# Performance work log

Measured on AMD Instinct MI355X. Metric: run time of the kernel, lower is better.

The kernel has to match this reference:

```python
import jax, jax.numpy as jnp
import numpy as np

B = 16384          # number of bags (offsets length)
L = 50             # indices per bag
N = B * L          # total flat indices
NUM_EMB = 10_000_000
DIM = 3


def setup_inputs() -> dict:
    key = jax.random.key(0)
    k_idx, k0, k1, k2 = jax.random.split(key, 4)
    eb_input = jax.random.randint(k_idx, (N,), 0, NUM_EMB, dtype=jnp.int64 if jax.config.jax_enable_x64 else jnp.int32)
    eb_offset = (jnp.arange(B) * L).astype(eb_input.dtype)  # sorted, starts at 0
    # 3 distinct tables (groups share one module object each in the original)
    table0 = jax.random.normal(k0, (NUM_EMB, DIM), dtype=jnp.float32)
    table1 = jax.random.normal(k1, (NUM_EMB, DIM), dtype=jnp.float32)
    table2 = jax.random.normal(k2, (NUM_EMB, DIM), dtype=jnp.float32)
    return {"eb_input": eb_input, "eb_offset": eb_offset,
            "table0": table0, "table1": table1, "table2": table2}


def _bag_sum(table, idx, seg_ids, num_bags):
    # gather rows then segment-sum -> EmbeddingBag(mode='sum')
    return jax.ops.segment_sum(table[idx], seg_ids, num_segments=num_bags)


def reference(eb_input, eb_offset, table0, table1, table2):
    n = eb_input.shape[0]
    num_bags = eb_offset.shape[0]
    # map each flat index position to its bag id
    seg_ids = jnp.searchsorted(eb_offset, jnp.arange(n, dtype=eb_offset.dtype), side='right') - 1
    p0 = _bag_sum(table0, eb_input, seg_ids, num_bags)  # [B, 3]
    p1 = _bag_sum(table1, eb_input, seg_ids, num_bags)
    p2 = _bag_sum(table2, eb_input, seg_ids, num_bags)
    # groups repeat the same bag 5 / 10 / 6 times, then cat along dim 0
    out = jnp.concatenate([
        jnp.tile(p0, (5, 1)),   # [5B, 3]
        jnp.tile(p1, (10, 1)),  # [10B, 3]
        jnp.tile(p2, (6, 1)),   # [6B, 3]
    ], axis=0)                   # [21B, 3]
    return out
```

## Files before the change

### kernel.cpp

```cpp
#include <hip/hip_runtime.h>


__device__ __forceinline__ float wave_reduce_sum(float v) {
#pragma unroll
    for (int off = 32; off > 0; off >>= 1)
        v += __shfl_down(v, off, 64);
    return v;
}

__global__ __launch_bounds__(256) void bag_sum_kernel(
    const int* __restrict__ eb_input,
    const int* __restrict__ eb_offset,
    const float* __restrict__ t0,
    const float* __restrict__ t1,
    const float* __restrict__ t2,
    float* __restrict__ out,
    int N, int B)
{
    const int wave = (blockIdx.x * blockDim.x + threadIdx.x) >> 6;
    const int lane = threadIdx.x & 63;
    if (wave >= B) return;

    const int start = eb_offset[wave];
    const int end   = (wave + 1 < B) ? eb_offset[wave + 1] : N;

    float s0x = 0.f, s0y = 0.f, s0z = 0.f;
    float s1x = 0.f, s1y = 0.f, s1z = 0.f;
    float s2x = 0.f, s2y = 0.f, s2z = 0.f;

    for (int i = start + lane; i < end; i += 64) {
        const long long j = (long long)eb_input[i] * 3;
        const float* __restrict__ p0 = t0 + j;
        const float* __restrict__ p1 = t1 + j;
        const float* __restrict__ p2 = t2 + j;
        s0x += p0[0]; s0y += p0[1]; s0z += p0[2];
        s1x += p1[0]; s1y += p1[1]; s1z += p1[2];
        s2x += p2[0]; s2y += p2[1]; s2z += p2[2];
    }

    s0x = wave_reduce_sum(s0x); s0y = wave_reduce_sum(s0y); s0z = wave_reduce_sum(s0z);
    s1x = wave_reduce_sum(s1x); s1y = wave_reduce_sum(s1y); s1z = wave_reduce_sum(s1z);
    s2x = wave_reduce_sum(s2x); s2y = wave_reduce_sum(s2y); s2z = wave_reduce_sum(s2z);

    if (lane == 0) {
        const size_t b = (size_t)wave;
        float* o0 = out + b * 3;
        float* o1 = out + ((size_t)5  * B + b) * 3;
        float* o2 = out + ((size_t)15 * B + b) * 3;
        o0[0] = s0x; o0[1] = s0y; o0[2] = s0z;
        o1[0] = s1x; o1[1] = s1y; o1[2] = s1z;
        o2[0] = s2x; o2[1] = s2y; o2[2] = s2z;
    }
}

__global__ __launch_bounds__(256) void tile_kernel(float* __restrict__ out, int B)
{
    const int r = blockIdx.x * blockDim.x + threadIdx.x;
    const int total = 18 * B;
    if (r >= total) return;

    size_t dst, src;
    if (r < 4 * B) {
        dst = (size_t)B + r;
        src = (size_t)(r % B);
    } else if (r < 13 * B) {
        const int q = r - 4 * B;
        dst = (size_t)6 * B + q;
        src = (size_t)5 * B + (q % B);
    } else {
        const int q = r - 13 * B;
        dst = (size_t)16 * B + q;
        src = (size_t)15 * B + (q % B);
    }

    const float* __restrict__ s = out + src * 3;
    float* __restrict__ d = out + dst * 3;
    const float a = s[0], b = s[1], c = s[2];
    d[0] = a; d[1] = b; d[2] = c;
}

extern "C" void kernel_launch(void* const* d_in, const int* in_sizes, int n_in,
                              void* d_out, int out_size, void* d_ws, size_t ws_size,
                              hipStream_t stream)
{
    const int*   eb_input  = (const int*)d_in[0];
    const int*   eb_offset = (const int*)d_in[1];
    const float* t0        = (const float*)d_in[2];
    const float* t1        = (const float*)d_in[3];
    const float* t2        = (const float*)d_in[4];
    float*       out       = (float*)d_out;

    const int N = in_sizes[0];
    const int B = in_sizes[1];

    const int blocksA = (B + 3) / 4;
    bag_sum_kernel<<<blocksA, 256, 0, stream>>>(eb_input, eb_offset, t0, t1, t2, out, N, B);

    const int totalRows = 18 * B;
    const int blocksB = (totalRows + 255) / 256;
    tile_kernel<<<blocksB, 256, 0, stream>>>(out, B);
}
```

Measured before the change: 59.19 us.

## Fuse bag-sum and tiling into one kernel with half-wave per bag

Merges the gather/sum kernel and the separate tile-copy kernel into a single launch. Each half-wave (32 lanes) now handles one bag, which suits the 50-index bags better than a full 64-lane wave. A butterfly xor reduction leaves the sum in every lane, so 21 lanes each write one replicated output row directly. This removes the second launch and the read-back of the output for tiling. Index math moves to 32-bit unsigned byte offsets, which overflow if index*12 exceeds 4 GB (fine for 10M rows).

```diff
diff --git a/kernel.cpp b/kernel.cpp
--- a/kernel.cpp
+++ b/kernel.cpp
@@ -1,14 +1,7 @@
 #include <hip/hip_runtime.h>
 
 
-__device__ __forceinline__ float wave_reduce_sum(float v) {
-#pragma unroll
-    for (int off = 32; off > 0; off >>= 1)
-        v += __shfl_down(v, off, 64);
-    return v;
-}
-
-__global__ __launch_bounds__(256) void bag_sum_kernel(
+__global__ __launch_bounds__(256) void bag_fused_kernel(
     const int* __restrict__ eb_input,
     const int* __restrict__ eb_offset,
     const float* __restrict__ t0,
@@ -17,66 +10,51 @@
     float* __restrict__ out,
     int N, int B)
 {
-    const int wave = (blockIdx.x * blockDim.x + threadIdx.x) >> 6;
+    const int wid  = (blockIdx.x * blockDim.x + threadIdx.x) >> 6;
     const int lane = threadIdx.x & 63;
-    if (wave >= B) return;
+    const int l5   = lane & 31;
+    const int b    = wid * 2 + (lane >> 5);
+    if (b >= B) return;
 
-    const int start = eb_offset[wave];
-    const int end   = (wave + 1 < B) ? eb_offset[wave + 1] : N;
+    const int start = eb_offset[b];
+    const int end   = (b + 1 < B) ? eb_offset[b + 1] : N;
 
     float s0x = 0.f, s0y = 0.f, s0z = 0.f;
     float s1x = 0.f, s1y = 0.f, s1z = 0.f;
     float s2x = 0.f, s2y = 0.f, s2z = 0.f;
 
-    for (int i = start + lane; i < end; i += 64) {
-        const long long j = (long long)eb_input[i] * 3;
-        const float* __restrict__ p0 = t0 + j;
-        const float* __restrict__ p1 = t1 + j;
-        const float* __restrict__ p2 = t2 + j;
+    for (int i = start + l5; i < end; i += 32) {
+        const unsigned idx = (unsigned)eb_input[i];
+        const size_t byteoff = (size_t)(idx * 12u);
+        const float* __restrict__ p0 = (const float*)((const char*)t0 + byteoff);
+        const float* __restrict__ p1 = (const float*)((const char*)t1 + byteoff);
+        const float* __restrict__ p2 = (const float*)((const char*)t2 + byteoff);
         s0x += p0[0]; s0y += p0[1]; s0z += p0[2];
         s1x += p1[0]; s1y += p1[1]; s1z += p1[2];
         s2x += p2[0]; s2y += p2[1]; s2z += p2[2];
     }
 
-    s0x = wave_reduce_sum(s0x); s0y = wave_reduce_sum(s0y); s0z = wave_reduce_sum(s0z);
-    s1x = wave_reduce_sum(s1x); s1y = wave_reduce_sum(s1y); s1z = wave_reduce_sum(s1z);
-    s2x = wave_reduce_sum(s2x); s2y = wave_reduce_sum(s2y); s2z = wave_reduce_sum(s2z);
-
-    if (lane == 0) {
-        const size_t b = (size_t)wave;
-        float* o0 = out + b * 3;
-        float* o1 = out + ((size_t)5  * B + b) * 3;
-        float* o2 = out + ((size_t)15 * B + b) * 3;
-        o0[0] = s0x; o0[1] = s0y; o0[2] = s0z;
-        o1[0] = s1x; o1[1] = s1y; o1[2] = s1z;
-        o2[0] = s2x; o2[1] = s2y; o2[2] = s2z;
-    }
-}
-
-__global__ __launch_bounds__(256) void tile_kernel(float* __restrict__ out, int B)
-{
-    const int r = blockIdx.x * blockDim.x + threadIdx.x;
-    const int total = 18 * B;
-    if (r >= total) return;
-
-    size_t dst, src;
-    if (r < 4 * B) {
-        dst = (size_t)B + r;
-        src = (size_t)(r % B);
-    } else if (r < 13 * B) {
-        const int q = r - 4 * B;
-        dst = (size_t)6 * B + q;
-        src = (size_t)5 * B + (q % B);
-    } else {
-        const int q = r - 13 * B;
-        dst = (size_t)16 * B + q;
-        src = (size_t)15 * B + (q % B);
+#pragma unroll
+    for (int off = 16; off > 0; off >>= 1) {
+        s0x += __shfl_xor(s0x, off, 64);
+        s0y += __shfl_xor(s0y, off, 64);
+        s0z += __shfl_xor(s0z, off, 64);
+        s1x += __shfl_xor(s1x, off, 64);
+        s1y += __shfl_xor(s1y, off, 64);
+        s1z += __shfl_xor(s1z, off, 64);
+        s2x += __shfl_xor(s2x, off, 64);
+        s2y += __shfl_xor(s2y, off, 64);
+        s2z += __shfl_xor(s2z, off, 64);
     }
 
-    const float* __restrict__ s = out + src * 3;
-    float* __restrict__ d = out + dst * 3;
-    const float a = s[0], b = s[1], c = s[2];
-    d[0] = a; d[1] = b; d[2] = c;
+    if (l5 < 21) {
+        float x, y, z;
+        if (l5 < 5)       { x = s0x; y = s0y; z = s0z; }
+        else if (l5 < 15) { x = s1x; y = s1y; z = s1z; }
+        else              { x = s2x; y = s2y; z = s2z; }
+        float* __restrict__ d = out + ((size_t)l5 * B + b) * 3;
+        d[0] = x; d[1] = y; d[2] = z;
+    }
 }
 
 extern "C" void kernel_launch(void* const* d_in, const int* in_sizes, int n_in,
@@ -93,10 +71,7 @@
     const int N = in_sizes[0];
     const int B = in_sizes[1];
 
-    const int blocksA = (B + 3) / 4;
-    bag_sum_kernel<<<blocksA, 256, 0, stream>>>(eb_input, eb_offset, t0, t1, t2, out, N, B);
-
-    const int totalRows = 18 * B;
-    const int blocksB = (totalRows + 255) / 256;
-    tile_kernel<<<blocksB, 256, 0, stream>>>(out, B);
+    const int waves  = (B + 1) / 2;
+    const int blocks = (waves + 3) / 4;
+    bag_fused_kernel<<<blocks, 256, 0, stream>>>(eb_input, eb_offset, t0, t1, t2, out, N, B);
 }
```

Result: faster. 57.55 us, median of 2 (-2.8%).
